# Optimization experiments

Hardware: AMD Instinct MI355X
Metric: run time of the kernel (lower is better)

Reference implementation:

```python
import jax, jax.numpy as jnp
import numpy as np

N = 100000   # nodes
E = 1600000  # edges (avg degree 16)
F_IN, F_HID, F_OUT = 64, 64, 16


def setup_inputs() -> dict:
    key = jax.random.key(0)
    ks = jax.random.split(key, 10)
    features = jax.random.normal(ks[0], (N, F_IN), dtype=jnp.float32)
    src = jax.random.randint(ks[1], (E,), 0, N, dtype=jnp.int32)
    dst = jax.random.randint(ks[2], (E,), 0, N, dtype=jnp.int32)
    # Xavier-uniform weights, zero bias (matches nn.init in the module)
    def xavier(k, fan_in, fan_out):
        lim = np.sqrt(6.0 / (fan_in + fan_out))
        return jax.random.uniform(k, (fan_in, fan_out), jnp.float32, -lim, lim)
    return {
        "features": features,
        "W1": xavier(ks[3], F_IN, F_HID), "b1": jnp.zeros((F_HID,), jnp.float32),
        "W2": xavier(ks[4], F_HID, F_HID), "b2": jnp.zeros((F_HID,), jnp.float32),
        "W3": xavier(ks[5], F_HID, F_OUT), "b3": jnp.zeros((F_OUT,), jnp.float32),
        "src": src, "dst": dst,
    }


def pairnorm_scs(x):
    # PairNorm 'PN-SCS', scale=1
    col_mean = x.mean(axis=0)                                    # [F]
    rownorm = jnp.sqrt(1e-6 + jnp.sum(x * x, axis=1, keepdims=True))  # [N,1]
    return x / rownorm - col_mean


def graph_conv(h, src, dst, W, b):
    # copy_u('h','m') + sum reduce over edges, plus self-loop
    agg = jax.ops.segment_sum(h[src], dst, num_segments=N) + h   # [N,F]
    return agg @ W + b


def reference(features, W1, b1, W2, b2, W3, b3, src, dst):
    h = features
    for W, b in ((W1, b1), (W2, b2)):
        h = pairnorm_scs(h)
        h = jax.nn.relu(graph_conv(h, src, dst, W, b))
        # dropout p=0.0 -> identity
    return graph_conv(h, src, dst, W3, b3)
```

## Files before the change

### kernel.cpp

```cpp
#include <hip/hip_runtime.h>
#include <hip/hip_fp8.h>


#define NHB 128

typedef float floatx2 __attribute__((ext_vector_type(2)));

__device__ __forceinline__ float rlane(float v, int k) {
  return __builtin_bit_cast(
      float, __builtin_amdgcn_readlane(__builtin_bit_cast(int, v), k));
}
__device__ __forceinline__ unsigned char f2fp8(float f) {
  __hip_fp8_e4m3 t(f);
  return (unsigned char)t.__x;
}
__device__ __forceinline__ float fp8tof(unsigned v) {
#if __has_builtin(__builtin_amdgcn_cvt_f32_fp8)
  return __builtin_amdgcn_cvt_f32_fp8((int)v, 0);
#else
  const unsigned h = ((v << 8) & 0x8000u) | ((v << 7) & 0x3f80u);
  __half_raw hr; hr.x = (unsigned short)h;
  return (float)__half(hr) * 256.0f;
#endif
}
__device__ __forceinline__ floatx2 fp8x2tof(unsigned short p) {
#if __has_builtin(__builtin_amdgcn_cvt_pk_f32_fp8)
  return __builtin_amdgcn_cvt_pk_f32_fp8((int)(unsigned)p, false);
#else
  floatx2 r; r.x = fp8tof(p & 0xffu); r.y = fp8tof(p >> 8); return r;
#endif
}

__global__ __launch_bounds__(256) void prelude_kernel(
    const int* __restrict__ dst, int* __restrict__ cntA, int E,
    const float* __restrict__ x, float* __restrict__ cs, int n4) {
  __shared__ int lc[NHB];
  __shared__ float lds[16][64];
  const int t = threadIdx.x;
  if (t < NHB) lc[t] = 0;
  __syncthreads();
  const int stride = gridDim.x * blockDim.x;
  for (int e = blockIdx.x * blockDim.x + t; e < E; e += stride)
    atomicAdd(&lc[__builtin_nontemporal_load(&dst[e]) >> 10], 1);

  float s0 = 0.f, s1 = 0.f, s2 = 0.f, s3 = 0.f;
  for (int i = blockIdx.x * blockDim.x + t; i < n4; i += stride) {
    float4 v = ((const float4*)x)[i];
    s0 += v.x; s1 += v.y; s2 += v.z; s3 += v.w;
  }
  const int r = t >> 4;
  const int cq = (t & 15) * 4;
  lds[r][cq + 0] = s0; lds[r][cq + 1] = s1; lds[r][cq + 2] = s2; lds[r][cq + 3] = s3;
  __syncthreads();
  if (t < NHB && lc[t]) atomicAdd(&cntA[t], lc[t]);
  if (t < 64) {
    float tot = 0.f;
    #pragma unroll
    for (int rr = 0; rr < 16; ++rr) tot += lds[rr][t];
    unsafeAtomicAdd(&cs[t], tot);
  }
}

__global__ __launch_bounds__(256) void matnorm_kernel(
    const float* x, const float* __restrict__ W,
    const float* __restrict__ cs, unsigned char* __restrict__ z,
    int N, float invN) {
  const int lane = threadIdx.x & 63;
  const int wid  = blockIdx.x * (blockDim.x >> 6) + (threadIdx.x >> 6);
  const int nw   = gridDim.x * (blockDim.x >> 6);

  float w[64];
  float cm0 = 0.f, cm1 = 0.f, cm2 = 0.f, cm3 = 0.f;
  #pragma unroll
  for (int k = 0; k < 64; k += 4) {
    w[k + 0] = W[(k + 0) * 64 + lane];
    w[k + 1] = W[(k + 1) * 64 + lane];
    w[k + 2] = W[(k + 2) * 64 + lane];
    w[k + 3] = W[(k + 3) * 64 + lane];
    cm0 = fmaf(cs[k + 0], w[k + 0], cm0);
    cm1 = fmaf(cs[k + 1], w[k + 1], cm1);
    cm2 = fmaf(cs[k + 2], w[k + 2], cm2);
    cm3 = fmaf(cs[k + 3], w[k + 3], cm3);
  }
  const float cm = ((cm0 + cm1) + (cm2 + cm3)) * invN;

  for (int row = wid; row < N; row += nw) {
    const float xv = x[(size_t)row * 64 + lane];
    float ss = xv * xv;
    #pragma unroll
    for (int m = 1; m < 64; m <<= 1) ss += __shfl_xor(ss, m, 64);
    const float rinv = 1.0f / sqrtf(1e-6f + ss);
    float a0 = 0.f, a1 = 0.f, a2 = 0.f, a3 = 0.f;
    #pragma unroll
    for (int k = 0; k < 64; k += 4) {
      a0 = fmaf(rlane(xv, k + 0), w[k + 0], a0);
      a1 = fmaf(rlane(xv, k + 1), w[k + 1], a1);
      a2 = fmaf(rlane(xv, k + 2), w[k + 2], a2);
      a3 = fmaf(rlane(xv, k + 3), w[k + 3], a3);
    }
    const float acc = (a0 + a1) + (a2 + a3);
    z[(size_t)row * 64 + lane] = f2fp8(acc * rinv - cm);
  }
}

__global__ __launch_bounds__(256) void matnorm2_kernel(
    const float* x, const float* __restrict__ W,
    float* __restrict__ cs, unsigned char* __restrict__ z, int N) {
  __shared__ float lred[4][64];
  const int lane = threadIdx.x & 63;
  const int wv   = threadIdx.x >> 6;
  const int wid  = blockIdx.x * (blockDim.x >> 6) + wv;
  const int nw   = gridDim.x * (blockDim.x >> 6);

  float w[64];
  #pragma unroll
  for (int k = 0; k < 64; k += 4) {
    w[k + 0] = W[(k + 0) * 64 + lane];
    w[k + 1] = W[(k + 1) * 64 + lane];
    w[k + 2] = W[(k + 2) * 64 + lane];
    w[k + 3] = W[(k + 3) * 64 + lane];
  }

  float csum = 0.f;
  for (int row = wid; row < N; row += nw) {
    const float xv = x[(size_t)row * 64 + lane];
    csum += xv;
    float ss = xv * xv;
    #pragma unroll
    for (int m = 1; m < 64; m <<= 1) ss += __shfl_xor(ss, m, 64);
    const float rinv = 1.0f / sqrtf(1e-6f + ss);
    float a0 = 0.f, a1 = 0.f, a2 = 0.f, a3 = 0.f;
    #pragma unroll
    for (int k = 0; k < 64; k += 4) {
      a0 = fmaf(rlane(xv, k + 0), w[k + 0], a0);
      a1 = fmaf(rlane(xv, k + 1), w[k + 1], a1);
      a2 = fmaf(rlane(xv, k + 2), w[k + 2], a2);
      a3 = fmaf(rlane(xv, k + 3), w[k + 3], a3);
    }
    const float acc = (a0 + a1) + (a2 + a3);
    z[(size_t)row * 64 + lane] = f2fp8(acc * rinv);
  }
  lred[wv][lane] = csum;
  __syncthreads();
  if (threadIdx.x < 64) {
    const float tot = lred[0][lane] + lred[1][lane] + lred[2][lane] + lred[3][lane];
    unsafeAtomicAdd(&cs[lane], tot);
  }
}

__global__ void cm2_kernel(const float* __restrict__ cs,
                           const float* __restrict__ W,
                           float* __restrict__ cm2, float invN) {
  const int m = threadIdx.x;
  float a0 = 0.f, a1 = 0.f, a2 = 0.f, a3 = 0.f;
  #pragma unroll
  for (int k = 0; k < 64; k += 4) {
    a0 = fmaf(cs[k + 0], W[(k + 0) * 64 + m], a0);
    a1 = fmaf(cs[k + 1], W[(k + 1) * 64 + m], a1);
    a2 = fmaf(cs[k + 2], W[(k + 2) * 64 + m], a2);
    a3 = fmaf(cs[k + 3], W[(k + 3) * 64 + m], a3);
  }
  cm2[m] = ((a0 + a1) + (a2 + a3)) * invN;
}


__global__ void scanA_kernel(const int* __restrict__ cntA,
                             int* __restrict__ baseA, int* __restrict__ curA,
                             int NHI) {
  __shared__ int s[NHB];
  const int t = threadIdx.x;
  const int v = (t < NHI) ? cntA[t] : 0;
  s[t] = v;
  __syncthreads();
  int acc = v;
  for (int off = 1; off < NHB; off <<= 1) {
    const int add = (t >= off) ? s[t - off] : 0;
    __syncthreads();
    acc += add;
    s[t] = acc;
    __syncthreads();
  }
  const int excl = acc - v;
  if (t < NHI) { baseA[t] = excl; curA[t] = excl; }
  if (t == NHI - 1) baseA[NHI] = acc;
}

#define TILE 2048
#define CAPA 48
__global__ __launch_bounds__(256) void scatterA_kernel(
    const int* __restrict__ src, const int* __restrict__ dst,
    int* __restrict__ curA, unsigned* __restrict__ ppack, int E) {
  __shared__ unsigned lpk[NHB][CAPA];
  __shared__ int lcnt[NHB], lbase[NHB];
  const int t = threadIdx.x;
  if (t < NHB) lcnt[t] = 0;
  __syncthreads();
  const int ntiles = (E + TILE - 1) / TILE;
  for (int tile = blockIdx.x; tile < ntiles; tile += gridDim.x) {
    const int base = tile * TILE;
    #pragma unroll
    for (int j = 0; j < TILE / 256; ++j) {
      const int e = base + j * 256 + t;
      if (e < E) {
        const int d = __builtin_nontemporal_load(&dst[e]);
        const int s = __builtin_nontemporal_load(&src[e]);
        const unsigned pw = ((unsigned)s << 10) | ((unsigned)d & 1023u);
        const int p = d >> 10;
        const int slot = atomicAdd(&lcnt[p], 1);
        if (slot < CAPA) lpk[p][slot] = pw;
        else ppack[atomicAdd(&curA[p], 1)] = pw;
      }
    }
    __syncthreads();
    if (t < NHB) {
      int c = lcnt[t]; if (c > CAPA) c = CAPA;
      lbase[t] = c ? atomicAdd(&curA[t], c) : 0;
      lcnt[t] = c;
    }
    __syncthreads();
    for (int p = 0; p < NHB; ++p) {
      const int c = lcnt[p];
      if (t < c) ppack[lbase[p] + t] = lpk[p][t];
    }
    __syncthreads();
    if (t < NHB) lcnt[t] = 0;
    __syncthreads();
  }
}

__global__ __launch_bounds__(512) void fillsort_kernel(
    const unsigned* __restrict__ ppack, const int* __restrict__ baseA,
    int* __restrict__ rowstart, int* __restrict__ csr, int N, int E) {
  __shared__ int hist[512];
  __shared__ int bs[512];
  const int t = threadIdx.x;
  const int hb = blockIdx.x;
  const int parent = hb >> 1;
  const unsigned half = (unsigned)(hb & 1);
  const int nlo = hb << 9;
  const int elo = baseA[parent], ehi = baseA[parent + 1];

  hist[t] = 0;
  __syncthreads();

  int e = elo + t;
  for (; e + 3 * 512 < ehi; e += 4 * 512) {
    const unsigned p0 = ppack[e],           p1 = ppack[e + 512];
    const unsigned p2 = ppack[e + 2 * 512], p3 = ppack[e + 3 * 512];
    if (((p0 >> 9) & 1u) == half) atomicAdd(&hist[p0 & 511u], 1);
    if (((p1 >> 9) & 1u) == half) atomicAdd(&hist[p1 & 511u], 1);
    if (((p2 >> 9) & 1u) == half) atomicAdd(&hist[p2 & 511u], 1);
    if (((p3 >> 9) & 1u) == half) atomicAdd(&hist[p3 & 511u], 1);
  }
  for (; e < ehi; e += 512) {
    const unsigned p = ppack[e];
    if (((p >> 9) & 1u) == half) atomicAdd(&hist[p & 511u], 1);
  }
  __syncthreads();

  const int c = hist[t];
  bs[t] = c;
  __syncthreads();
  for (int off = 1; off < 512; off <<= 1) {
    const int v = (t >= off) ? bs[t - off] : 0;
    __syncthreads();
    bs[t] += v;
    __syncthreads();
  }
  const int excl = bs[t] - c;
  const int total = bs[511];
  const int halfbase = half ? (ehi - total) : elo;

  hist[t] = excl;
  const int n0 = nlo + t;
  if (n0 < N) rowstart[n0] = halfbase + excl;
  if (hb == 0 && t == 0) rowstart[N] = E;
  __syncthreads();

  e = elo + t;
  for (; e + 3 * 512 < ehi; e += 4 * 512) {
    const unsigned p0 = ppack[e],           p1 = ppack[e + 512];
    const unsigned p2 = ppack[e + 2 * 512], p3 = ppack[e + 3 * 512];
    if (((p0 >> 9) & 1u) == half)
      csr[halfbase + atomicAdd(&hist[p0 & 511u], 1)] = (int)(p0 >> 10);
    if (((p1 >> 9) & 1u) == half)
      csr[halfbase + atomicAdd(&hist[p1 & 511u], 1)] = (int)(p1 >> 10);
    if (((p2 >> 9) & 1u) == half)
      csr[halfbase + atomicAdd(&hist[p2 & 511u], 1)] = (int)(p2 >> 10);
    if (((p3 >> 9) & 1u) == half)
      csr[halfbase + atomicAdd(&hist[p3 & 511u], 1)] = (int)(p3 >> 10);
  }
  for (; e < ehi; e += 512) {
    const unsigned p = ppack[e];
    if (((p >> 9) & 1u) == half)
      csr[halfbase + atomicAdd(&hist[p & 511u], 1)] = (int)(p >> 10);
  }
}

__global__ __launch_bounds__(256) void gather64_kernel(
    const unsigned char* __restrict__ z, const float* __restrict__ b,
    const int* __restrict__ rowstart, const int* __restrict__ csr,
    float* __restrict__ agg, int N) {
  const int lane = threadIdx.x & 63;
  const int h    = lane >> 5;
  const int il   = lane & 31;
  const int f0   = il << 1;
  const int pair = blockIdx.x * (blockDim.x >> 6) + (threadIdx.x >> 6);
  const int n0 = pair << 1;
  if (n0 >= N) return;
  const int node = n0 + h;
  const bool hv = (node < N);
  const int start = hv ? rowstart[node] : 0;
  const int end   = hv ? rowstart[node + 1] : 0;
  const int deg   = end - start;
  const int degA = __builtin_amdgcn_readfirstlane(deg);
  const int degB = __builtin_amdgcn_readlane(deg, 32);
  const int maxdeg = degA > degB ? degA : degB;

  const unsigned char* zp = z + f0;
  const unsigned short sv =
      hv ? *(const unsigned short*)(zp + (size_t)node * 64) : (unsigned short)0;

  float a00 = 0.f, a01 = 0.f, a10 = 0.f, a11 = 0.f;
  for (int w0 = 0; w0 < maxdeg; w0 += 32) {
    const int ei = start + w0 + il;
    const int safe = (ei < end) ? ei : (end > start ? end - 1 : 0);
    const int cidx = csr[safe];
    const int rem = maxdeg - w0;
    const int nloc = rem < 32 ? rem : 32;
    int j0 = 0;
    for (; j0 + 16 <= nloc; j0 += 16) {
      int idx[16];
      #pragma unroll
      for (int j = 0; j < 16; ++j)
        idx[j] = __shfl(cidx, (h << 5) + j0 + j, 64);
      unsigned short hh[16];
      #pragma unroll
      for (int j = 0; j < 16; ++j)
        hh[j] = *(const unsigned short*)(zp + (size_t)(unsigned)idx[j] * 64u);
      #pragma unroll
      for (int j = 0; j < 16; ++j) {
        const unsigned short m = (w0 + j0 + j < deg) ? hh[j] : (unsigned short)0;
        const floatx2 v = fp8x2tof(m);
        if (j & 1) { a10 += v.x; a11 += v.y; }
        else       { a00 += v.x; a01 += v.y; }
      }
    }
    for (; j0 + 4 <= nloc; j0 += 4) {
      int idx[4];
      #pragma unroll
      for (int j = 0; j < 4; ++j)
        idx[j] = __shfl(cidx, (h << 5) + j0 + j, 64);
      unsigned short hh[4];
      #pragma unroll
      for (int j = 0; j < 4; ++j)
        hh[j] = *(const unsigned short*)(zp + (size_t)(unsigned)idx[j] * 64u);
      #pragma unroll
      for (int j = 0; j < 4; ++j) {
        const unsigned short m = (w0 + j0 + j < deg) ? hh[j] : (unsigned short)0;
        const floatx2 v = fp8x2tof(m);
        if (j & 1) { a10 += v.x; a11 += v.y; }
        else       { a00 += v.x; a01 += v.y; }
      }
    }
    for (; j0 < nloc; ++j0) {
      const int idx = __shfl(cidx, (h << 5) + j0, 64);
      const unsigned short hh =
          *(const unsigned short*)(zp + (size_t)(unsigned)idx * 64u);
      const unsigned short m = (w0 + j0 < deg) ? hh : (unsigned short)0;
      const floatx2 v = fp8x2tof(m);
      a00 += v.x; a01 += v.y;
    }
  }
  if (hv) {
    const floatx2 sf = fp8x2tof(sv);
    const float2 bb = *(const float2*)(b + f0);
    float2 st;
    st.x = fmaxf(sf.x + bb.x + a00 + a10, 0.f);
    st.y = fmaxf(sf.y + bb.y + a01 + a11, 0.f);
    *(float2*)(agg + (size_t)node * 64 + f0) = st;
  }
}

__global__ __launch_bounds__(256) void gather_l2_kernel(
    const unsigned char* __restrict__ z2, const float* __restrict__ b2,
    const float* __restrict__ W3, const float* __restrict__ cm2,
    const int* __restrict__ rowstart, const int* __restrict__ csr,
    unsigned char* __restrict__ z3, int N) {
  const int lane = threadIdx.x & 63;
  int node = blockIdx.x * (blockDim.x >> 6) + (threadIdx.x >> 6);
  if (node >= N) return;
  node = __builtin_amdgcn_readfirstlane(node);
  float4 w4[4];
  #pragma unroll
  for (int q = 0; q < 4; ++q)
    w4[q] = ((const float4*)(W3 + lane * 16))[q];
  const float cml = cm2[lane];

  const int start = rowstart[node];
  const int end   = rowstart[node + 1];
  const unsigned char hs = z2[(size_t)node * 64 + lane];
  float a0 = 0.f, a1 = 0.f, a2 = 0.f, a3 = 0.f;
  int e = start;
  for (; e + 16 <= end; e += 16) {
    unsigned char h[16];
    #pragma unroll
    for (int j = 0; j < 16; ++j) h[j] = z2[(size_t)csr[e + j] * 64 + lane];
    #pragma unroll
    for (int j = 0; j < 16; j += 4) {
      a0 += fp8tof(h[j + 0]); a1 += fp8tof(h[j + 1]);
      a2 += fp8tof(h[j + 2]); a3 += fp8tof(h[j + 3]);
    }
  }
  for (; e + 4 <= end; e += 4) {
    unsigned char h[4];
    #pragma unroll
    for (int j = 0; j < 4; ++j) h[j] = z2[(size_t)csr[e + j] * 64 + lane];
    a0 += fp8tof(h[0]); a1 += fp8tof(h[1]); a2 += fp8tof(h[2]); a3 += fp8tof(h[3]);
  }
  for (; e < end; ++e) a0 += fp8tof(z2[(size_t)csr[e] * 64 + lane]);
  const float sum = (a0 + a1) + (a2 + a3);
  const float corr = (float)(end - start + 1) * cml;
  const float o = fmaxf(fp8tof(hs) + b2[lane] + sum - corr, 0.f);

  float p[16];
  #pragma unroll
  for (int q = 0; q < 4; ++q) {
    p[4 * q + 0] = o * w4[q].x;
    p[4 * q + 1] = o * w4[q].y;
    p[4 * q + 2] = o * w4[q].z;
    p[4 * q + 3] = o * w4[q].w;
  }
  {
    const bool up = (lane & 1);
    #pragma unroll
    for (int m = 0; m < 8; ++m) {
      const float mine = up ? p[m + 8] : p[m];
      const float give = up ? p[m] : p[m + 8];
      p[m] = mine + __shfl_xor(give, 1, 64);
    }
  }
  {
    const bool up = (lane & 2);
    #pragma unroll
    for (int m = 0; m < 4; ++m) {
      const float mine = up ? p[m + 4] : p[m];
      const float give = up ? p[m] : p[m + 4];
      p[m] = mine + __shfl_xor(give, 2, 64);
    }
  }
  {
    const bool up = (lane & 4);
    #pragma unroll
    for (int m = 0; m < 2; ++m) {
      const float mine = up ? p[m + 2] : p[m];
      const float give = up ? p[m] : p[m + 2];
      p[m] = mine + __shfl_xor(give, 4, 64);
    }
  }
  {
    const bool up = (lane & 8);
    const float mine = up ? p[1] : p[0];
    const float give = up ? p[0] : p[1];
    p[0] = mine + __shfl_xor(give, 8, 64);
  }
  p[0] += __shfl_xor(p[0], 16, 64);
  p[0] += __shfl_xor(p[0], 32, 64);

  if (lane < 16) {
    const int j = ((lane & 1) << 3) | ((lane & 2) << 1) |
                  ((lane & 4) >> 1) | ((lane & 8) >> 3);
    z3[(size_t)node * 16 + j] = f2fp8(p[0]);
  }
}

__global__ __launch_bounds__(256) void gather16_kernel(
    const unsigned char* __restrict__ z3, const float* __restrict__ b3,
    const int* __restrict__ rowstart, const int* __restrict__ csr,
    float* __restrict__ out, int N) {
  const int lane = threadIdx.x & 63;
  const int f = lane & 15;
  const int g = lane >> 4;
  int node = blockIdx.x * (blockDim.x >> 6) + (threadIdx.x >> 6);
  if (node >= N) return;
  node = __builtin_amdgcn_readfirstlane(node);
  const int start = rowstart[node];
  const int end   = rowstart[node + 1];
  float acc0 = 0.f, acc1 = 0.f;
  int e = start + g;
  for (; e + 4 < end; e += 8) {
    acc0 += fp8tof(z3[(size_t)csr[e] * 16 + f]);
    acc1 += fp8tof(z3[(size_t)csr[e + 4] * 16 + f]);
  }
  if (e < end) acc0 += fp8tof(z3[(size_t)csr[e] * 16 + f]);
  float acc = acc0 + acc1;
  acc += __shfl_xor(acc, 16, 64);
  acc += __shfl_xor(acc, 32, 64);
  if (lane < 16)
    out[(size_t)node * 16 + f] = fp8tof(z3[(size_t)node * 16 + f]) + b3[f] + acc;
}

extern "C" void kernel_launch(void* const* d_in, const int* in_sizes, int n_in,
                              void* d_out, int out_size, void* d_ws, size_t ws_size,
                              hipStream_t stream) {
  const float* feat = (const float*)d_in[0];
  const float* W1 = (const float*)d_in[1];
  const float* b1 = (const float*)d_in[2];
  const float* W2 = (const float*)d_in[3];
  const float* b2 = (const float*)d_in[4];
  const float* W3 = (const float*)d_in[5];
  const float* b3 = (const float*)d_in[6];
  const int* src = (const int*)d_in[7];
  const int* dst = (const int*)d_in[8];
  const int N = in_sizes[0] / 64;
  const int E = in_sizes[7];
  float* out = (float*)d_out;

  float* B            = (float*)d_ws;
  unsigned char* zb   = (unsigned char*)(B + (size_t)N * 64);
  unsigned char* z3b  = zb + (size_t)N * 64;
  int* cntA  = (int*)(z3b + (size_t)N * 16);
  float* cs1 = (float*)(cntA + NHB);
  float* cs2 = cs1 + 64;
  float* cm2w = cs2 + 64;
  int* baseA    = (int*)(cm2w + 64);
  int* curA     = baseA + NHB + 1;
  int* rowstart = curA + NHB;
  int* csr      = rowstart + N + 1;
  unsigned* ppack = (unsigned*)zb;

  const int NHI = (N + 1023) >> 10;
  const int node_blocks = (N + 3) / 4;
  const int npairs = (N + 1) / 2;
  const int pair_blocks = (npairs + 3) / 4;
  const float invN = 1.0f / (float)N;

  hipMemsetAsync(cntA, 0, (NHB + 128) * sizeof(int), stream);
  prelude_kernel<<<512, 256, 0, stream>>>(dst, cntA, E, feat, cs1, N * 16);
  scanA_kernel<<<1, NHB, 0, stream>>>(cntA, baseA, curA, NHI);
  scatterA_kernel<<<512, 256, 0, stream>>>(src, dst, curA, ppack, E);
  fillsort_kernel<<<2 * NHI, 512, 0, stream>>>(ppack, baseA, rowstart, csr, N, E);

  matnorm_kernel<<<1024, 256, 0, stream>>>(feat, W1, cs1, zb, N, invN);
  gather64_kernel<<<pair_blocks, 256, 0, stream>>>(zb, b1, rowstart, csr, B, N);

  matnorm2_kernel<<<1024, 256, 0, stream>>>(B, W2, cs2, zb, N);
  cm2_kernel<<<1, 64, 0, stream>>>(cs2, W2, cm2w, invN);
  gather_l2_kernel<<<node_blocks, 256, 0, stream>>>(zb, b2, W3, cm2w, rowstart,
                                                    csr, z3b, N);

  gather16_kernel<<<node_blocks, 256, 0, stream>>>(z3b, b3, rowstart, csr, out, N);
}
```

Measured before the change: 368.7 us.

## Split layer-2 gather into pair-per-wave gather and separate W3 matmul kernel

The layer-2 aggregation now uses the two-nodes-per-wavefront layout already used by gather64: each lane handles two features, loads edge indices cooperatively, and shares them with shuffles. The result is written as bf16 to an intermediate buffer. A new w3mat kernel then reads that buffer and applies W3 to produce the fp8 z3. This removes the per-lane serial csr loads and the one-byte gathers of the old fused kernel. The cost is an extra launch and a round trip of the intermediate through memory, plus bf16 rounding of the hidden activations.

```diff
diff --git a/kernel.cpp b/kernel.cpp
--- a/kernel.cpp
+++ b/kernel.cpp
@@ -6,6 +6,14 @@
 
 typedef float floatx2 __attribute__((ext_vector_type(2)));
 
+__device__ __forceinline__ unsigned short f2bf(float f) {
+  unsigned u = __builtin_bit_cast(unsigned, f);
+  u += 0x7FFFu + ((u >> 16) & 1u);
+  return (unsigned short)(u >> 16);
+}
+__device__ __forceinline__ float bf2f(unsigned short h) {
+  return __builtin_bit_cast(float, ((unsigned)h) << 16);
+}
 __device__ __forceinline__ float rlane(float v, int k) {
   return __builtin_bit_cast(
       float, __builtin_amdgcn_readlane(__builtin_bit_cast(int, v), k));
@@ -384,8 +392,93 @@
 
 __global__ __launch_bounds__(256) void gather_l2_kernel(
     const unsigned char* __restrict__ z2, const float* __restrict__ b2,
-    const float* __restrict__ W3, const float* __restrict__ cm2,
-    const int* __restrict__ rowstart, const int* __restrict__ csr,
+    const float* __restrict__ cm2, const int* __restrict__ rowstart,
+    const int* __restrict__ csr, unsigned* __restrict__ o, int N) {
+  const int lane = threadIdx.x & 63;
+  const int h    = lane >> 5;
+  const int il   = lane & 31;
+  const int f0   = il << 1;
+  const int pair = blockIdx.x * (blockDim.x >> 6) + (threadIdx.x >> 6);
+  const int n0 = pair << 1;
+  if (n0 >= N) return;
+  const int node = n0 + h;
+  const bool hv = (node < N);
+  const int start = hv ? rowstart[node] : 0;
+  const int end   = hv ? rowstart[node + 1] : 0;
+  const int deg   = end - start;
+  const int degA = __builtin_amdgcn_readfirstlane(deg);
+  const int degB = __builtin_amdgcn_readlane(deg, 32);
+  const int maxdeg = degA > degB ? degA : degB;
+
+  const unsigned char* zp = z2 + f0;
+  const unsigned short sv =
+      hv ? *(const unsigned short*)(zp + (size_t)node * 64) : (unsigned short)0;
+
+  float a00 = 0.f, a01 = 0.f, a10 = 0.f, a11 = 0.f;
+  for (int w0 = 0; w0 < maxdeg; w0 += 32) {
+    const int ei = start + w0 + il;
+    const int safe = (ei < end) ? ei : (end > start ? end - 1 : 0);
+    const int cidx = csr[safe];
+    const int rem = maxdeg - w0;
+    const int nloc = rem < 32 ? rem : 32;
+    int j0 = 0;
+    for (; j0 + 16 <= nloc; j0 += 16) {
+      int idx[16];
+      #pragma unroll
+      for (int j = 0; j < 16; ++j)
+        idx[j] = __shfl(cidx, (h << 5) + j0 + j, 64);
+      unsigned short hh[16];
+      #pragma unroll
+      for (int j = 0; j < 16; ++j)
+        hh[j] = *(const unsigned short*)(zp + (size_t)(unsigned)idx[j] * 64u);
+      #pragma unroll
+      for (int j = 0; j < 16; ++j) {
+        const unsigned short m = (w0 + j0 + j < deg) ? hh[j] : (unsigned short)0;
+        const floatx2 v = fp8x2tof(m);
+        if (j & 1) { a10 += v.x; a11 += v.y; }
+        else       { a00 += v.x; a01 += v.y; }
+      }
+    }
+    for (; j0 + 4 <= nloc; j0 += 4) {
+      int idx[4];
+      #pragma unroll
+      for (int j = 0; j < 4; ++j)
+        idx[j] = __shfl(cidx, (h << 5) + j0 + j, 64);
+      unsigned short hh[4];
+      #pragma unroll
+      for (int j = 0; j < 4; ++j)
+        hh[j] = *(const unsigned short*)(zp + (size_t)(unsigned)idx[j] * 64u);
+      #pragma unroll
+      for (int j = 0; j < 4; ++j) {
+        const unsigned short m = (w0 + j0 + j < deg) ? hh[j] : (unsigned short)0;
+        const floatx2 v = fp8x2tof(m);
+        if (j & 1) { a10 += v.x; a11 += v.y; }
+        else       { a00 += v.x; a01 += v.y; }
+      }
+    }
+    for (; j0 < nloc; ++j0) {
+      const int idx = __shfl(cidx, (h << 5) + j0, 64);
+      const unsigned short hh =
+          *(const unsigned short*)(zp + (size_t)(unsigned)idx * 64u);
+      const unsigned short m = (w0 + j0 < deg) ? hh : (unsigned short)0;
+      const floatx2 v = fp8x2tof(m);
+      a00 += v.x; a01 += v.y;
+    }
+  }
+  if (hv) {
+    const floatx2 sf = fp8x2tof(sv);
+    const float2 bb = *(const float2*)(b2 + f0);
+    const float2 cc = *(const float2*)(cm2 + f0);
+    const float dp1 = (float)(deg + 1);
+    const float o0 = fmaxf(sf.x + bb.x + (a00 + a10) - dp1 * cc.x, 0.f);
+    const float o1 = fmaxf(sf.y + bb.y + (a01 + a11) - dp1 * cc.y, 0.f);
+    o[(size_t)node * 32 + il] =
+        (unsigned)f2bf(o0) | ((unsigned)f2bf(o1) << 16);
+  }
+}
+
+__global__ __launch_bounds__(256) void w3mat_kernel(
+    const unsigned short* __restrict__ o16, const float* __restrict__ W3,
     unsigned char* __restrict__ z3, int N) {
   const int lane = threadIdx.x & 63;
   int node = blockIdx.x * (blockDim.x >> 6) + (threadIdx.x >> 6);
@@ -395,33 +488,7 @@
   #pragma unroll
   for (int q = 0; q < 4; ++q)
     w4[q] = ((const float4*)(W3 + lane * 16))[q];
-  const float cml = cm2[lane];
-
-  const int start = rowstart[node];
-  const int end   = rowstart[node + 1];
-  const unsigned char hs = z2[(size_t)node * 64 + lane];
-  float a0 = 0.f, a1 = 0.f, a2 = 0.f, a3 = 0.f;
-  int e = start;
-  for (; e + 16 <= end; e += 16) {
-    unsigned char h[16];
-    #pragma unroll
-    for (int j = 0; j < 16; ++j) h[j] = z2[(size_t)csr[e + j] * 64 + lane];
-    #pragma unroll
-    for (int j = 0; j < 16; j += 4) {
-      a0 += fp8tof(h[j + 0]); a1 += fp8tof(h[j + 1]);
-      a2 += fp8tof(h[j + 2]); a3 += fp8tof(h[j + 3]);
-    }
-  }
-  for (; e + 4 <= end; e += 4) {
-    unsigned char h[4];
-    #pragma unroll
-    for (int j = 0; j < 4; ++j) h[j] = z2[(size_t)csr[e + j] * 64 + lane];
-    a0 += fp8tof(h[0]); a1 += fp8tof(h[1]); a2 += fp8tof(h[2]); a3 += fp8tof(h[3]);
-  }
-  for (; e < end; ++e) a0 += fp8tof(z2[(size_t)csr[e] * 64 + lane]);
-  const float sum = (a0 + a1) + (a2 + a3);
-  const float corr = (float)(end - start + 1) * cml;
-  const float o = fmaxf(fp8tof(hs) + b2[lane] + sum - corr, 0.f);
+  const float o = bf2f(o16[(size_t)node * 64 + lane]);
 
   float p[16];
   #pragma unroll
@@ -528,6 +595,7 @@
   int* rowstart = curA + NHB;
   int* csr      = rowstart + N + 1;
   unsigned* ppack = (unsigned*)zb;
+  unsigned* ob = (unsigned*)B;
 
   const int NHI = (N + 1023) >> 10;
   const int node_blocks = (N + 3) / 4;
@@ -546,8 +614,10 @@
 
   matnorm2_kernel<<<1024, 256, 0, stream>>>(B, W2, cs2, zb, N);
   cm2_kernel<<<1, 64, 0, stream>>>(cs2, W2, cm2w, invN);
-  gather_l2_kernel<<<node_blocks, 256, 0, stream>>>(zb, b2, W3, cm2w, rowstart,
-                                                    csr, z3b, N);
+  gather_l2_kernel<<<pair_blocks, 256, 0, stream>>>(zb, b2, cm2w, rowstart, csr,
+                                                    ob, N);
+  w3mat_kernel<<<node_blocks, 256, 0, stream>>>((const unsigned short*)ob, W3,
+                                                z3b, N);
 
   gather16_kernel<<<node_blocks, 256, 0, stream>>>(z3b, b3, rowstart, csr, out, N);
 }
```

Result: faster. 361.3 us, median of 2 (-2.0%).
